# Performance work log

Measured on AMD Instinct MI355X. Metric: run time of the kernel, lower is better.

The kernel has to match this reference:

```python
import jax, jax.numpy as jnp
import numpy as np

N, IN_C, HEADS, OUT_C = 4096, 256, 4, 64
NEG_SLOPE = 0.2


def setup_inputs() -> dict:
    key = jax.random.key(0)
    k1, k2, k3, k4, k5 = jax.random.split(key, 5)
    x = jax.random.normal(k1, (N, IN_C), dtype=jnp.float32)
    adj = jax.random.randint(k2, (N, N), 0, 2, dtype=jnp.int32)
    # xavier-uniform style scales
    s_w = float(np.sqrt(6.0 / (IN_C + HEADS * OUT_C)))
    s_a = float(np.sqrt(6.0 / (HEADS + OUT_C)))
    W = jax.random.uniform(k3, (IN_C, HEADS * OUT_C), jnp.float32, -s_w, s_w)
    att_l = jax.random.uniform(k4, (HEADS, OUT_C), jnp.float32, -s_a, s_a)
    att_r = jax.random.uniform(k5, (HEADS, OUT_C), jnp.float32, -s_a, s_a)
    bias = jnp.zeros((HEADS * OUT_C,), jnp.float32)
    return {"x": x, "adj": adj, "W": W, "att_l": att_l, "att_r": att_r, "bias": bias}


def reference(x, adj, W, att_l, att_r, bias):
    n = x.shape[0]
    h = (x @ W).reshape(n, HEADS, OUT_C)              # [N, H, C]
    el = jnp.einsum('nhc,hc->nh', h, att_l)           # [N, H]
    er = jnp.einsum('nhc,hc->nh', h, att_r)           # [N, H]
    e = el[:, None, :] + er[None, :, :]               # [N, N, H]
    e = jnp.where(e >= 0, e, NEG_SLOPE * e)           # leaky_relu
    mask = (adj > 0)[:, :, None]                      # [N, N, 1]
    e = jnp.where(mask, e, -jnp.inf)
    alpha = jax.nn.softmax(e, axis=1)                 # softmax over j
    out = jnp.einsum('ijh,jhc->ihc', alpha, h)        # [N, H, C]
    out = out.reshape(n, HEADS * OUT_C) + bias
    return out
```

## Files before the change

kernel.cpp:

```cpp
#include <hip/hip_runtime.h>
#include <hip/hip_bf16.h>
#include <stdint.h>

typedef float f32x4 __attribute__((ext_vector_type(4)));
typedef short s16x8 __attribute__((ext_vector_type(8)));
typedef int   i32x4 __attribute__((ext_vector_type(4)));
typedef unsigned int u32;

#define NNODES 4096
#define INC    256
#define OUTF   256
#define NEG    0.2f

__device__ __forceinline__ unsigned short f2bf(float f) {
  unsigned u = __float_as_uint(f);
  u += 0x7FFFu + ((u >> 16) & 1u);
  return (unsigned short)(u >> 16);
}
__device__ __forceinline__ unsigned encf(float x) {
  unsigned u = __float_as_uint(x);
  return (u & 0x80000000u) ? ~u : (u | 0x80000000u);
}
__device__ __forceinline__ float decf(unsigned e) {
  unsigned u = (e & 0x80000000u) ? (e ^ 0x80000000u) : ~e;
  return __uint_as_float(u);
}

__global__ __launch_bounds__(256) void k_feat(
    const float* __restrict__ x, const float* __restrict__ W,
    const float* __restrict__ attl, const float* __restrict__ attr,
    unsigned short* __restrict__ hT, float* __restrict__ el_t,
    u32* __restrict__ QS, unsigned* __restrict__ M_enc)
{
  __shared__ float sm[4352];
  float* xs  = sm;
  float* wsl = sm + 2176;
  const int tid = threadIdx.x;
  const int hb = blockIdx.x, nb = blockIdx.y;
  const int n0 = nb * 64, c0 = hb * 64;
  const int ty = tid >> 4, tx = tid & 15;

  float acc[4][4];
#pragma unroll
  for (int r = 0; r < 4; ++r)
#pragma unroll
    for (int j = 0; j < 4; ++j) acc[r][j] = 0.f;

  const int sn = tid >> 2, sko = (tid & 3) * 8;
  const int wk = tid >> 3, wco = (tid & 7) * 8;

  for (int kc = 0; kc < INC; kc += 32) {
    __syncthreads();
    {
      const float* xp = x + (size_t)(n0 + sn) * INC + kc + sko;
      float4 a = *(const float4*)xp;
      float4 b = *(const float4*)(xp + 4);
      xs[(sko + 0) * 68 + sn] = a.x; xs[(sko + 1) * 68 + sn] = a.y;
      xs[(sko + 2) * 68 + sn] = a.z; xs[(sko + 3) * 68 + sn] = a.w;
      xs[(sko + 4) * 68 + sn] = b.x; xs[(sko + 5) * 68 + sn] = b.y;
      xs[(sko + 6) * 68 + sn] = b.z; xs[(sko + 7) * 68 + sn] = b.w;
      const float* wp = W + (size_t)(kc + wk) * OUTF + c0 + wco;
      *(float4*)(wsl + wk * 68 + wco)     = *(const float4*)wp;
      *(float4*)(wsl + wk * 68 + wco + 4) = *(const float4*)(wp + 4);
    }
    __syncthreads();
#pragma unroll
    for (int k = 0; k < 32; ++k) {
      float4 a = *(const float4*)(xs + k * 68 + ty * 4);
      float4 b = *(const float4*)(wsl + k * 68 + tx * 4);
      acc[0][0] = fmaf(a.x, b.x, acc[0][0]); acc[0][1] = fmaf(a.x, b.y, acc[0][1]);
      acc[0][2] = fmaf(a.x, b.z, acc[0][2]); acc[0][3] = fmaf(a.x, b.w, acc[0][3]);
      acc[1][0] = fmaf(a.y, b.x, acc[1][0]); acc[1][1] = fmaf(a.y, b.y, acc[1][1]);
      acc[1][2] = fmaf(a.y, b.z, acc[1][2]); acc[1][3] = fmaf(a.y, b.w, acc[1][3]);
      acc[2][0] = fmaf(a.z, b.x, acc[2][0]); acc[2][1] = fmaf(a.z, b.y, acc[2][1]);
      acc[2][2] = fmaf(a.z, b.z, acc[2][2]); acc[2][3] = fmaf(a.z, b.w, acc[2][3]);
      acc[3][0] = fmaf(a.w, b.x, acc[3][0]); acc[3][1] = fmaf(a.w, b.y, acc[3][1]);
      acc[3][2] = fmaf(a.w, b.z, acc[3][2]); acc[3][3] = fmaf(a.w, b.w, acc[3][3]);
    }
  }

  float4 al = *(const float4*)(attl + c0 + tx * 4);
  float4 ar = *(const float4*)(attr + c0 + tx * 4);
  float pl[4], pr[4];
#pragma unroll
  for (int r = 0; r < 4; ++r) {
    pl[r] = acc[r][0] * al.x + acc[r][1] * al.y + acc[r][2] * al.z + acc[r][3] * al.w;
    pr[r] = acc[r][0] * ar.x + acc[r][1] * ar.y + acc[r][2] * ar.z + acc[r][3] * ar.w;
  }
#pragma unroll
  for (int m = 1; m < 16; m <<= 1) {
#pragma unroll
    for (int r = 0; r < 4; ++r) {
      pl[r] += __shfl_xor(pl[r], m, 64);
      pr[r] += __shfl_xor(pr[r], m, 64);
    }
  }
  if (tx == 0) {
#pragma unroll
    for (int r = 0; r < 4; ++r) {
      el_t[hb * NNODES + n0 + ty * 4 + r] = pl[r];
      float q = __expf(pr[r]);
      float s = __expf(NEG * pr[r]);
      QS[hb * NNODES + n0 + ty * 4 + r] = (u32)f2bf(q) | ((u32)f2bf(s) << 16);
    }
  }
  float mx = fmaxf(fmaxf(pr[0], pr[1]), fmaxf(pr[2], pr[3]));
  mx = fmaxf(mx, __shfl_xor(mx, 16, 64));
  mx = fmaxf(mx, __shfl_xor(mx, 32, 64));
  if ((tid & 63) == 0) atomicMax(M_enc + hb, encf(mx));

  __syncthreads();
#pragma unroll
  for (int r = 0; r < 4; ++r)
#pragma unroll
    for (int j = 0; j < 4; ++j)
      sm[(tx * 4 + j) * 68 + ty * 4 + r] = acc[r][j];
  __syncthreads();
  {
    const int c = tid >> 2, ns = (tid & 3) * 16;
    unsigned v[8];
#pragma unroll
    for (int i = 0; i < 8; ++i) {
      unsigned lo = f2bf(sm[c * 68 + ns + 2 * i]);
      unsigned hi = f2bf(sm[c * 68 + ns + 2 * i + 1]);
      v[i] = lo | (hi << 16);
    }
    const int sw = (c & 3) ^ ((c >> 2) & 3);
    const int blk = n0 + (ns & 32);
    const int g0 = (ns & 16) >> 3;
    unsigned short* dstb = hT + (size_t)(c0 + c) * NNODES + blk;
    *(uint4*)(dstb + ((g0 ^ sw) * 8))       = make_uint4(v[0], v[1], v[2], v[3]);
    *(uint4*)(dstb + (((g0 + 1) ^ sw) * 8)) = make_uint4(v[4], v[5], v[6], v[7]);
  }
}

__global__ __launch_bounds__(256, 2) void k_gat(
    const int* __restrict__ adj, const unsigned short* __restrict__ hT,
    const float* __restrict__ el_t, const u32* __restrict__ QS,
    const unsigned* __restrict__ M_enc,
    float* __restrict__ nump, float* __restrict__ denp, int jlen)
{
  __shared__ __align__(16) unsigned short hbuf[4][8192];
  __shared__ __align__(16) u32 qbuf[4][128];
  const int tid = threadIdx.x;
  const int wid = tid >> 6, lane = tid & 63;
  const int l15 = lane & 15, lg = lane >> 4;
  const int i0 = (blockIdx.x * 4 + wid) * 16;
  const int js = blockIdx.y;
  const int j0 = js * jlen;
  const int irow = i0 + l15;
  const int sw_l = (l15 & 3) ^ ((l15 >> 2) & 3);

  float P[4], Rr[4];
#pragma unroll
  for (int h = 0; h < 4; ++h) {
    float el  = el_t[h * NNODES + irow];
    float M   = decf(M_enc[h]);
    float sE  = el + M;
    float mih = fmaxf(sE, NEG * sE);
    P[h]  = __expf(el - mih);
    Rr[h] = __expf(NEG * el - mih);
  }

  const unsigned short* hsrc = hT + (size_t)(wid * 64 + (lane >> 2)) * NNODES + j0 + (lane & 3) * 8;
  const u32*            qsrc = QS + (size_t)(lane >> 5) * NNODES + j0 + (lane & 31);
  const int*            asrc = adj + (size_t)irow * NNODES + j0 + lg * 8;

  f32x4 acc[4][4];
  f32x4 accd[4];
#pragma unroll
  for (int h = 0; h < 4; ++h) {
    accd[h] = (f32x4){0.f, 0.f, 0.f, 0.f};
#pragma unroll
    for (int c = 0; c < 4; ++c) acc[h][c] = (f32x4){0.f, 0.f, 0.f, 0.f};
  }
  s16x8 ones;
#pragma unroll
  for (int e = 0; e < 8; ++e) ones[e] = (short)0x3F80;

  const int niter = jlen >> 5;

#define FILL(T, SLOT)                                                            \
  do {                                                                           \
    const unsigned short* hs_ = hsrc + (size_t)(T) * 32;                         \
    _Pragma("unroll")                                                            \
    for (int q_ = 0; q_ < 4; ++q_)                                               \
      __builtin_amdgcn_global_load_lds(hs_ + (size_t)q_ * 16 * NNODES,           \
                                       &hbuf[SLOT][wid * 2048 + q_ * 512], 16, 0, 0); \
    const u32* qs_ = qsrc + (size_t)(T) * 32;                                    \
    __builtin_amdgcn_global_load_lds(qs_,              &qbuf[SLOT][0],  4, 0, 0);\
    __builtin_amdgcn_global_load_lds(qs_ + 2 * NNODES, &qbuf[SLOT][64], 4, 0, 0);\
  } while (0)

  FILL(0, 0);
  i32x4 ac0 = *(const i32x4*)(asrc);
  i32x4 ac1 = *(const i32x4*)(asrc + 4);
  const int t1 = (niter > 1) ? 1 : 0;
  FILL(t1, 1);
  i32x4 an0 = *(const i32x4*)(asrc + (size_t)t1 * 32);
  i32x4 an1 = *(const i32x4*)(asrc + (size_t)t1 * 32 + 4);

  for (int k = 0; k < niter; ++k) {
    const int t2 = (k + 2 < niter) ? (k + 2) : (niter - 1);
    FILL(t2, (k + 2) & 3);
    asm volatile("s_waitcnt vmcnt(14)" ::: "memory");
    const int* ap = asrc + (size_t)t2 * 32;
    i32x4 af0 = *(const i32x4*)(ap);
    i32x4 af1 = *(const i32x4*)(ap + 4);
    __builtin_amdgcn_s_barrier();

    const int cs = k & 3;
#pragma unroll
    for (int h = 0; h < 4; ++h) {
      const unsigned short* lb = &hbuf[cs][(h * 64 + l15) * 32 + ((lg ^ sw_l) * 8)];
      s16x8 b0 = *(const s16x8*)(lb);
      s16x8 b1 = *(const s16x8*)(lb + 16 * 32);
      s16x8 b2 = *(const s16x8*)(lb + 32 * 32);
      s16x8 b3 = *(const s16x8*)(lb + 48 * 32);
      const u32* qrow = &qbuf[cs][h * 32 + lg * 8];
      i32x4 q0 = *(const i32x4*)(qrow);
      i32x4 q1 = *(const i32x4*)(qrow + 4);

      float w[8];
#pragma unroll
      for (int e = 0; e < 4; ++e) {
        u32 m0 = (ac0[e] > 0) ? (u32)q0[e] : 0u;
        u32 m1 = (ac1[e] > 0) ? (u32)q1[e] : 0u;
        float qq0 = __uint_as_float(m0 << 16);
        float ss0 = __uint_as_float(m0 & 0xffff0000u);
        float qq1 = __uint_as_float(m1 << 16);
        float ss1 = __uint_as_float(m1 & 0xffff0000u);
        w[e]     = fmaxf(P[h] * qq0, Rr[h] * ss0);
        w[e + 4] = fmaxf(P[h] * qq1, Rr[h] * ss1);
      }
      union { u32 uu[4]; s16x8 v; } af;
#pragma unroll
      for (int p = 0; p < 4; ++p)
        asm("v_cvt_pk_bf16_f32 %0, %1, %2" : "=v"(af.uu[p]) : "v"(w[2 * p]), "v"(w[2 * p + 1]));

      acc[h][0] = __builtin_amdgcn_mfma_f32_16x16x32_bf16(af.v, b0,   acc[h][0], 0, 0, 0);
      acc[h][1] = __builtin_amdgcn_mfma_f32_16x16x32_bf16(af.v, b1,   acc[h][1], 0, 0, 0);
      acc[h][2] = __builtin_amdgcn_mfma_f32_16x16x32_bf16(af.v, b2,   acc[h][2], 0, 0, 0);
      acc[h][3] = __builtin_amdgcn_mfma_f32_16x16x32_bf16(af.v, b3,   acc[h][3], 0, 0, 0);
      accd[h]   = __builtin_amdgcn_mfma_f32_16x16x32_bf16(af.v, ones, accd[h],   0, 0, 0);
    }

    ac0 = an0; ac1 = an1; an0 = af0; an1 = af1;
  }
#undef FILL

  const int orow = i0 + lg * 4;
  float* np = nump + ((size_t)js * NNODES + orow) * OUTF + l15;
#pragma unroll
  for (int h = 0; h < 4; ++h)
#pragma unroll
    for (int c = 0; c < 4; ++c)
#pragma unroll
      for (int r = 0; r < 4; ++r)
        np[r * OUTF + h * 64 + c * 16] = acc[h][c][r];

  if (l15 == 0) {
    float* dp = denp + ((size_t)js * NNODES + orow) * 4;
#pragma unroll
    for (int h = 0; h < 4; ++h)
#pragma unroll
      for (int r = 0; r < 4; ++r) dp[r * 4 + h] = accd[h][r];
  }
}

__global__ __launch_bounds__(256) void k_div(
    const float* __restrict__ nump, const float* __restrict__ denp,
    const float* __restrict__ bias, float* __restrict__ out, int sj)
{
  const int q  = blockIdx.x * 256 + threadIdx.x;
  const int n  = q >> 6;
  const int c4 = (q & 63) * 4;
  const int h  = c4 >> 6;
  f32x4 s = {0.f, 0.f, 0.f, 0.f};
  float d = 0.f;
  for (int t = 0; t < sj; ++t) {
    s += *(const f32x4*)(nump + ((size_t)t * NNODES + n) * OUTF + c4);
    d += denp[((size_t)t * NNODES + n) * 4 + h];
  }
  f32x4 b = *(const f32x4*)(bias + c4);
  float r = __builtin_amdgcn_rcpf(d);
  f32x4 o = s * r + b;
  *(f32x4*)(out + (size_t)n * OUTF + c4) = o;
}

extern "C" void kernel_launch(void* const* d_in, const int* in_sizes, int n_in,
                              void* d_out, int out_size, void* d_ws, size_t ws_size,
                              hipStream_t stream)
{
  const float* x    = (const float*)d_in[0];
  const int*   adj  = (const int*)d_in[1];
  const float* W    = (const float*)d_in[2];
  const float* attl = (const float*)d_in[3];
  const float* attr = (const float*)d_in[4];
  const float* bias = (const float*)d_in[5];
  float* out = (float*)d_out;
  char*  ws  = (char*)d_ws;

  unsigned short* hT  = (unsigned short*)ws;
  float*    el_t  = (float*)(ws + (2u << 20));
  u32*      QS    = (u32*)(ws + (2u << 20) + (64u << 10));
  unsigned* M_enc = (unsigned*)(ws + (2u << 20) + (128u << 10));
  float*    denp  = (float*)(ws + (2u << 20) + (192u << 10));
  const size_t nbase = (3u << 20);

  const size_t per_split = (size_t)NNODES * OUTF * 4;
  int sj = 8;
  while (sj > 1 && ws_size < nbase + (size_t)sj * per_split) sj >>= 1;
  float* nump = (sj == 1) ? out : (float*)(ws + nbase);

  hipMemsetAsync(M_enc, 0, 16, stream);
  k_feat<<<dim3(4, 64), 256, 0, stream>>>(x, W, attl, attr, hT, el_t, QS, M_enc);
  k_gat<<<dim3(64, sj), 256, 0, stream>>>(adj, hT, el_t, QS, M_enc, nump, denp, NNODES / sj);
  k_div<<<dim3(1024), 256, 0, stream>>>(nump, denp, bias, out, sj);
}
```

Measured before the change: 74.09 us.

## Split GAT aggregation by head per wave and preload all attention scalars

The aggregation kernel now uses 512-thread blocks of 8 waves, with each wave owning one head for 16 rows instead of all four heads. This cuts per-wave accumulator registers and quadruples the number of waves available for latency hiding. The packed exp scalars for the whole 512-column slice are loaded into LDS once, and the adjacency prefetch becomes a 4-slot unrolled ring. The feature kernel is retiled to 32-row blocks for more blocks, and the split count is fixed at 8, which drops the fallback for a small workspace. In exchange, adjacency rows are now re-read by four waves per row group.

Result: slower. 96.10 us (+29.7%).

```diff
diff --git a/kernel.cpp b/kernel.cpp
--- a/kernel.cpp
+++ b/kernel.cpp
@@ -11,6 +11,9 @@
 #define INC    256
 #define OUTF   256
 #define NEG    0.2f
+#define SJ     8
+#define JL     512
+#define NIT    16
 
 __device__ __forceinline__ unsigned short f2bf(float f) {
   unsigned u = __float_as_uint(f);
@@ -32,239 +35,223 @@
     unsigned short* __restrict__ hT, float* __restrict__ el_t,
     u32* __restrict__ QS, unsigned* __restrict__ M_enc)
 {
-  __shared__ float sm[4352];
+  __shared__ float sm[3328];
   float* xs  = sm;
-  float* wsl = sm + 2176;
+  float* wsl = sm + 1152;
   const int tid = threadIdx.x;
   const int hb = blockIdx.x, nb = blockIdx.y;
-  const int n0 = nb * 64, c0 = hb * 64;
+  const int n0 = nb * 32, c0 = hb * 64;
   const int ty = tid >> 4, tx = tid & 15;
 
-  float acc[4][4];
-#pragma unroll
-  for (int r = 0; r < 4; ++r)
+  float acc[2][4];
+#pragma unroll
+  for (int r = 0; r < 2; ++r)
 #pragma unroll
     for (int j = 0; j < 4; ++j) acc[r][j] = 0.f;
 
-  const int sn = tid >> 2, sko = (tid & 3) * 8;
-  const int wk = tid >> 3, wco = (tid & 7) * 8;
+  const int sxn = tid >> 3;
+  const int sxk = (tid & 7) * 4;
+  const int swk = tid >> 3;
+  const int swc = (tid & 7) * 8;
 
   for (int kc = 0; kc < INC; kc += 32) {
     __syncthreads();
     {
-      const float* xp = x + (size_t)(n0 + sn) * INC + kc + sko;
-      float4 a = *(const float4*)xp;
-      float4 b = *(const float4*)(xp + 4);
-      xs[(sko + 0) * 68 + sn] = a.x; xs[(sko + 1) * 68 + sn] = a.y;
-      xs[(sko + 2) * 68 + sn] = a.z; xs[(sko + 3) * 68 + sn] = a.w;
-      xs[(sko + 4) * 68 + sn] = b.x; xs[(sko + 5) * 68 + sn] = b.y;
-      xs[(sko + 6) * 68 + sn] = b.z; xs[(sko + 7) * 68 + sn] = b.w;
-      const float* wp = W + (size_t)(kc + wk) * OUTF + c0 + wco;
-      *(float4*)(wsl + wk * 68 + wco)     = *(const float4*)wp;
-      *(float4*)(wsl + wk * 68 + wco + 4) = *(const float4*)(wp + 4);
+      float4 a = *(const float4*)(x + (size_t)(n0 + sxn) * INC + kc + sxk);
+      xs[(sxk + 0) * 36 + sxn] = a.x;
+      xs[(sxk + 1) * 36 + sxn] = a.y;
+      xs[(sxk + 2) * 36 + sxn] = a.z;
+      xs[(sxk + 3) * 36 + sxn] = a.w;
+      const float* wp = W + (size_t)(kc + swk) * OUTF + c0 + swc;
+      *(float4*)(wsl + swk * 68 + swc)     = *(const float4*)wp;
+      *(float4*)(wsl + swk * 68 + swc + 4) = *(const float4*)(wp + 4);
     }
     __syncthreads();
 #pragma unroll
     for (int k = 0; k < 32; ++k) {
-      float4 a = *(const float4*)(xs + k * 68 + ty * 4);
+      float a0 = xs[k * 36 + ty * 2];
+      float a1 = xs[k * 36 + ty * 2 + 1];
       float4 b = *(const float4*)(wsl + k * 68 + tx * 4);
-      acc[0][0] = fmaf(a.x, b.x, acc[0][0]); acc[0][1] = fmaf(a.x, b.y, acc[0][1]);
-      acc[0][2] = fmaf(a.x, b.z, acc[0][2]); acc[0][3] = fmaf(a.x, b.w, acc[0][3]);
-      acc[1][0] = fmaf(a.y, b.x, acc[1][0]); acc[1][1] = fmaf(a.y, b.y, acc[1][1]);
-      acc[1][2] = fmaf(a.y, b.z, acc[1][2]); acc[1][3] = fmaf(a.y, b.w, acc[1][3]);
-      acc[2][0] = fmaf(a.z, b.x, acc[2][0]); acc[2][1] = fmaf(a.z, b.y, acc[2][1]);
-      acc[2][2] = fmaf(a.z, b.z, acc[2][2]); acc[2][3] = fmaf(a.z, b.w, acc[2][3]);
-      acc[3][0] = fmaf(a.w, b.x, acc[3][0]); acc[3][1] = fmaf(a.w, b.y, acc[3][1]);
-      acc[3][2] = fmaf(a.w, b.z, acc[3][2]); acc[3][3] = fmaf(a.w, b.w, acc[3][3]);
+      acc[0][0] = fmaf(a0, b.x, acc[0][0]); acc[0][1] = fmaf(a0, b.y, acc[0][1]);
+      acc[0][2] = fmaf(a0, b.z, acc[0][2]); acc[0][3] = fmaf(a0, b.w, acc[0][3]);
+      acc[1][0] = fmaf(a1, b.x, acc[1][0]); acc[1][1] = fmaf(a1, b.y, acc[1][1]);
+      acc[1][2] = fmaf(a1, b.z, acc[1][2]); acc[1][3] = fmaf(a1, b.w, acc[1][3]);
     }
   }
 
   float4 al = *(const float4*)(attl + c0 + tx * 4);
   float4 ar = *(const float4*)(attr + c0 + tx * 4);
-  float pl[4], pr[4];
-#pragma unroll
-  for (int r = 0; r < 4; ++r) {
+  float pl[2], pr[2];
+#pragma unroll
+  for (int r = 0; r < 2; ++r) {
     pl[r] = acc[r][0] * al.x + acc[r][1] * al.y + acc[r][2] * al.z + acc[r][3] * al.w;
     pr[r] = acc[r][0] * ar.x + acc[r][1] * ar.y + acc[r][2] * ar.z + acc[r][3] * ar.w;
   }
 #pragma unroll
   for (int m = 1; m < 16; m <<= 1) {
 #pragma unroll
-    for (int r = 0; r < 4; ++r) {
+    for (int r = 0; r < 2; ++r) {
       pl[r] += __shfl_xor(pl[r], m, 64);
       pr[r] += __shfl_xor(pr[r], m, 64);
     }
   }
   if (tx == 0) {
 #pragma unroll
-    for (int r = 0; r < 4; ++r) {
-      el_t[hb * NNODES + n0 + ty * 4 + r] = pl[r];
+    for (int r = 0; r < 2; ++r) {
+      el_t[hb * NNODES + n0 + ty * 2 + r] = pl[r];
       float q = __expf(pr[r]);
       float s = __expf(NEG * pr[r]);
-      QS[hb * NNODES + n0 + ty * 4 + r] = (u32)f2bf(q) | ((u32)f2bf(s) << 16);
-    }
-  }
-  float mx = fmaxf(fmaxf(pr[0], pr[1]), fmaxf(pr[2], pr[3]));
+      QS[hb * NNODES + n0 + ty * 2 + r] = (u32)f2bf(q) | ((u32)f2bf(s) << 16);
+    }
+  }
+  float mx = fmaxf(pr[0], pr[1]);
   mx = fmaxf(mx, __shfl_xor(mx, 16, 64));
   mx = fmaxf(mx, __shfl_xor(mx, 32, 64));
   if ((tid & 63) == 0) atomicMax(M_enc + hb, encf(mx));
 
   __syncthreads();
 #pragma unroll
-  for (int r = 0; r < 4; ++r)
+  for (int r = 0; r < 2; ++r)
 #pragma unroll
     for (int j = 0; j < 4; ++j)
-      sm[(tx * 4 + j) * 68 + ty * 4 + r] = acc[r][j];
+      sm[(tx * 4 + j) * 33 + ty * 2 + r] = acc[r][j];
   __syncthreads();
   {
-    const int c = tid >> 2, ns = (tid & 3) * 16;
-    unsigned v[8];
-#pragma unroll
-    for (int i = 0; i < 8; ++i) {
-      unsigned lo = f2bf(sm[c * 68 + ns + 2 * i]);
-      unsigned hi = f2bf(sm[c * 68 + ns + 2 * i + 1]);
+    const int c = tid >> 2, g = tid & 3;
+    unsigned v[4];
+#pragma unroll
+    for (int i = 0; i < 4; ++i) {
+      unsigned lo = f2bf(sm[c * 33 + g * 8 + 2 * i]);
+      unsigned hi = f2bf(sm[c * 33 + g * 8 + 2 * i + 1]);
       v[i] = lo | (hi << 16);
     }
     const int sw = (c & 3) ^ ((c >> 2) & 3);
-    const int blk = n0 + (ns & 32);
-    const int g0 = (ns & 16) >> 3;
-    unsigned short* dstb = hT + (size_t)(c0 + c) * NNODES + blk;
-    *(uint4*)(dstb + ((g0 ^ sw) * 8))       = make_uint4(v[0], v[1], v[2], v[3]);
-    *(uint4*)(dstb + (((g0 + 1) ^ sw) * 8)) = make_uint4(v[4], v[5], v[6], v[7]);
-  }
-}
-
-__global__ __launch_bounds__(256, 2) void k_gat(
+    unsigned short* dst = hT + (size_t)(c0 + c) * NNODES + n0 + ((g ^ sw) * 8);
+    *(uint4*)dst = make_uint4(v[0], v[1], v[2], v[3]);
+  }
+}
+
+__global__ __launch_bounds__(512, 4) void k_gat(
     const int* __restrict__ adj, const unsigned short* __restrict__ hT,
     const float* __restrict__ el_t, const u32* __restrict__ QS,
     const unsigned* __restrict__ M_enc,
-    float* __restrict__ nump, float* __restrict__ denp, int jlen)
+    float* __restrict__ nump, float* __restrict__ denp)
 {
   __shared__ __align__(16) unsigned short hbuf[4][8192];
-  __shared__ __align__(16) u32 qbuf[4][128];
+  __shared__ __align__(16) u32 qsAll[4 * JL];
+
   const int tid = threadIdx.x;
   const int wid = tid >> 6, lane = tid & 63;
   const int l15 = lane & 15, lg = lane >> 4;
-  const int i0 = (blockIdx.x * 4 + wid) * 16;
+  const int h  = wid & 3;
+  const int ic = wid >> 2;
+  const int i0 = blockIdx.x * 32 + ic * 16;
   const int js = blockIdx.y;
-  const int j0 = js * jlen;
+  const int j0 = js * JL;
   const int irow = i0 + l15;
   const int sw_l = (l15 & 3) ^ ((l15 >> 2) & 3);
 
-  float P[4], Rr[4];
-#pragma unroll
-  for (int h = 0; h < 4; ++h) {
-    float el  = el_t[h * NNODES + irow];
-    float M   = decf(M_enc[h]);
-    float sE  = el + M;
-    float mih = fmaxf(sE, NEG * sE);
-    P[h]  = __expf(el - mih);
-    Rr[h] = __expf(NEG * el - mih);
-  }
-
-  const unsigned short* hsrc = hT + (size_t)(wid * 64 + (lane >> 2)) * NNODES + j0 + (lane & 3) * 8;
-  const u32*            qsrc = QS + (size_t)(lane >> 5) * NNODES + j0 + (lane & 31);
+  const float el = el_t[h * NNODES + irow];
+  const float M  = decf(M_enc[h]);
+  const float sE = el + M;
+  const float mih = fmaxf(sE, NEG * sE);
+  const float P = __expf(el - mih);
+  const float R = __expf(NEG * el - mih);
+
+  const unsigned short* hsrc = hT + (size_t)(wid * 16 + (lane >> 2)) * NNODES + j0 + (lane & 3) * 8;
   const int*            asrc = adj + (size_t)irow * NNODES + j0 + lg * 8;
 
-  f32x4 acc[4][4];
-  f32x4 accd[4];
-#pragma unroll
-  for (int h = 0; h < 4; ++h) {
-    accd[h] = (f32x4){0.f, 0.f, 0.f, 0.f};
-#pragma unroll
-    for (int c = 0; c < 4; ++c) acc[h][c] = (f32x4){0.f, 0.f, 0.f, 0.f};
-  }
+  {
+    const u32* qs_ = QS + (size_t)(wid >> 1) * NNODES + j0 + (wid & 1) * 256 + lane * 4;
+    __builtin_amdgcn_global_load_lds(qs_, &qsAll[wid * 256], 16, 0, 0);
+  }
+
+  f32x4 acc[4];
+  f32x4 accd = {0.f, 0.f, 0.f, 0.f};
+#pragma unroll
+  for (int c = 0; c < 4; ++c) acc[c] = (f32x4){0.f, 0.f, 0.f, 0.f};
   s16x8 ones;
 #pragma unroll
   for (int e = 0; e < 8; ++e) ones[e] = (short)0x3F80;
 
-  const int niter = jlen >> 5;
-
-#define FILL(T, SLOT)                                                            \
-  do {                                                                           \
+  i32x4 aS[4][2];
+
+#define HFILL(T, SLOT) do {                                                      \
     const unsigned short* hs_ = hsrc + (size_t)(T) * 32;                         \
-    _Pragma("unroll")                                                            \
-    for (int q_ = 0; q_ < 4; ++q_)                                               \
-      __builtin_amdgcn_global_load_lds(hs_ + (size_t)q_ * 16 * NNODES,           \
-                                       &hbuf[SLOT][wid * 2048 + q_ * 512], 16, 0, 0); \
-    const u32* qs_ = qsrc + (size_t)(T) * 32;                                    \
-    __builtin_amdgcn_global_load_lds(qs_,              &qbuf[SLOT][0],  4, 0, 0);\
-    __builtin_amdgcn_global_load_lds(qs_ + 2 * NNODES, &qbuf[SLOT][64], 4, 0, 0);\
+    __builtin_amdgcn_global_load_lds(hs_, &hbuf[SLOT][wid * 512], 16, 0, 0);     \
+    __builtin_amdgcn_global_load_lds(hs_ + (size_t)128 * NNODES,                 \
+                                     &hbuf[SLOT][4096 + wid * 512], 16, 0, 0);   \
   } while (0)
 
-  FILL(0, 0);
-  i32x4 ac0 = *(const i32x4*)(asrc);
-  i32x4 ac1 = *(const i32x4*)(asrc + 4);
-  const int t1 = (niter > 1) ? 1 : 0;
-  FILL(t1, 1);
-  i32x4 an0 = *(const i32x4*)(asrc + (size_t)t1 * 32);
-  i32x4 an1 = *(const i32x4*)(asrc + (size_t)t1 * 32 + 4);
-
-  for (int k = 0; k < niter; ++k) {
-    const int t2 = (k + 2 < niter) ? (k + 2) : (niter - 1);
-    FILL(t2, (k + 2) & 3);
-    asm volatile("s_waitcnt vmcnt(14)" ::: "memory");
-    const int* ap = asrc + (size_t)t2 * 32;
-    i32x4 af0 = *(const i32x4*)(ap);
-    i32x4 af1 = *(const i32x4*)(ap + 4);
-    __builtin_amdgcn_s_barrier();
-
-    const int cs = k & 3;
-#pragma unroll
-    for (int h = 0; h < 4; ++h) {
-      const unsigned short* lb = &hbuf[cs][(h * 64 + l15) * 32 + ((lg ^ sw_l) * 8)];
+  HFILL(0, 0);
+  aS[0][0] = *(const i32x4*)(asrc);
+  aS[0][1] = *(const i32x4*)(asrc + 4);
+  HFILL(1, 1);
+  aS[1][0] = *(const i32x4*)(asrc + 32);
+  aS[1][1] = *(const i32x4*)(asrc + 36);
+
+  for (int kb = 0; kb < NIT; kb += 4) {
+#pragma unroll
+    for (int u = 0; u < 4; ++u) {
+      const int k = kb + u;
+      const int t2 = (k + 2 < NIT) ? (k + 2) : (NIT - 1);
+      HFILL(t2, (u + 2) & 3);
+      {
+        const int* ap = asrc + t2 * 32;
+        aS[(u + 2) & 3][0] = *(const i32x4*)(ap);
+        aS[(u + 2) & 3][1] = *(const i32x4*)(ap + 4);
+      }
+      asm volatile("s_waitcnt vmcnt(8)" ::: "memory");
+      __builtin_amdgcn_s_barrier();
+
+      const unsigned short* lb = &hbuf[u][(h * 64 + l15) * 32 + ((lg ^ sw_l) * 8)];
       s16x8 b0 = *(const s16x8*)(lb);
       s16x8 b1 = *(const s16x8*)(lb + 16 * 32);
       s16x8 b2 = *(const s16x8*)(lb + 32 * 32);
       s16x8 b3 = *(const s16x8*)(lb + 48 * 32);
-      const u32* qrow = &qbuf[cs][h * 32 + lg * 8];
+      const u32* qrow = &qsAll[h * JL + k * 32 + lg * 8];
       i32x4 q0 = *(const i32x4*)(qrow);
       i32x4 q1 = *(const i32x4*)(qrow + 4);
 
+      const i32x4 a0 = aS[u][0], a1 = aS[u][1];
       float w[8];
 #pragma unroll
       for (int e = 0; e < 4; ++e) {
-        u32 m0 = (ac0[e] > 0) ? (u32)q0[e] : 0u;
-        u32 m1 = (ac1[e] > 0) ? (u32)q1[e] : 0u;
+        u32 m0 = (a0[e] > 0) ? (u32)q0[e] : 0u;
+        u32 m1 = (a1[e] > 0) ? (u32)q1[e] : 0u;
         float qq0 = __uint_as_float(m0 << 16);
         float ss0 = __uint_as_float(m0 & 0xffff0000u);
         float qq1 = __uint_as_float(m1 << 16);
         float ss1 = __uint_as_float(m1 & 0xffff0000u);
-        w[e]     = fmaxf(P[h] * qq0, Rr[h] * ss0);
-        w[e + 4] = fmaxf(P[h] * qq1, Rr[h] * ss1);
+        w[e]     = fmaxf(P * qq0, R * ss0);
+        w[e + 4] = fmaxf(P * qq1, R * ss1);
       }
       union { u32 uu[4]; s16x8 v; } af;
 #pragma unroll
       for (int p = 0; p < 4; ++p)
         asm("v_cvt_pk_bf16_f32 %0, %1, %2" : "=v"(af.uu[p]) : "v"(w[2 * p]), "v"(w[2 * p + 1]));
 
-      acc[h][0] = __builtin_amdgcn_mfma_f32_16x16x32_bf16(af.v, b0,   acc[h][0], 0, 0, 0);
-      acc[h][1] = __builtin_amdgcn_mfma_f32_16x16x32_bf16(af.v, b1,   acc[h][1], 0, 0, 0);
-      acc[h][2] = __builtin_amdgcn_mfma_f32_16x16x32_bf16(af.v, b2,   acc[h][2], 0, 0, 0);
-      acc[h][3] = __builtin_amdgcn_mfma_f32_16x16x32_bf16(af.v, b3,   acc[h][3], 0, 0, 0);
-      accd[h]   = __builtin_amdgcn_mfma_f32_16x16x32_bf16(af.v, ones, accd[h],   0, 0, 0);
-    }
-
-    ac0 = an0; ac1 = an1; an0 = af0; an1 = af1;
-  }
-#undef FILL
+      acc[0] = __builtin_amdgcn_mfma_f32_16x16x32_bf16(af.v, b0,   acc[0], 0, 0, 0);
+      acc[1] = __builtin_amdgcn_mfma_f32_16x16x32_bf16(af.v, b1,   acc[1], 0, 0, 0);
+      acc[2] = __builtin_amdgcn_mfma_f32_16x16x32_bf16(af.v, b2,   acc[2], 0, 0, 0);
+      acc[3] = __builtin_amdgcn_mfma_f32_16x16x32_bf16(af.v, b3,   acc[3], 0, 0, 0);
+      accd   = __builtin_amdgcn_mfma_f32_16x16x32_bf16(af.v, ones, accd,   0, 0, 0);
+    }
+  }
+#undef HFILL
 
   const int orow = i0 + lg * 4;
-  float* np = nump + ((size_t)js * NNODES + orow) * OUTF + l15;
-#pragma unroll
-  for (int h = 0; h < 4; ++h)
-#pragma unroll
-    for (int c = 0; c < 4; ++c)
-#pragma unroll
-      for (int r = 0; r < 4; ++r)
-        np[r * OUTF + h * 64 + c * 16] = acc[h][c][r];
+  float* np = nump + ((size_t)js * NNODES + orow) * OUTF + h * 64 + l15;
+#pragma unroll
+  for (int c = 0; c < 4; ++c)
+#pragma unroll
+    for (int r = 0; r < 4; ++r)
+      np[r * OUTF + c * 16] = acc[c][r];
 
   if (l15 == 0) {
-    float* dp = denp + ((size_t)js * NNODES + orow) * 4;
-#pragma unroll
-    for (int h = 0; h < 4; ++h)
-#pragma unroll
-      for (int r = 0; r < 4; ++r) dp[r * 4 + h] = accd[h][r];
+    float* dp = denp + ((size_t)js * NNODES + orow) * 4 + h;
+#pragma unroll
+    for (int r = 0; r < 4; ++r) dp[r * 4] = accd[r];
   }
 }
 
@@ -307,14 +294,10 @@
   unsigned* M_enc = (unsigned*)(ws + (2u << 20) + (128u << 10));
   float*    denp  = (float*)(ws + (2u << 20) + (192u << 10));
   const size_t nbase = (3u << 20);
-
-  const size_t per_split = (size_t)NNODES * OUTF * 4;
-  int sj = 8;
-  while (sj > 1 && ws_size < nbase + (size_t)sj * per_split) sj >>= 1;
-  float* nump = (sj == 1) ? out : (float*)(ws + nbase);
+  float* nump = (float*)(ws + nbase);
 
   hipMemsetAsync(M_enc, 0, 16, stream);
-  k_feat<<<dim3(4, 64), 256, 0, stream>>>(x, W, attl, attr, hT, el_t, QS, M_enc);
-  k_gat<<<dim3(64, sj), 256, 0, stream>>>(adj, hT, el_t, QS, M_enc, nump, denp, NNODES / sj);
-  k_div<<<dim3(1024), 256, 0, stream>>>(nump, denp, bias, out, sj);
-}
+  k_feat<<<dim3(4, 128), 256, 0, stream>>>(x, W, attl, attr, hT, el_t, QS, M_enc);
+  k_gat<<<dim3(128, SJ), 512, 0, stream>>>(adj, hT, el_t, QS, M_enc, nump, denp);
+  k_div<<<dim3(1024), 256, 0, stream>>>(nump, denp, bias, out, SJ);
+}
```
